# Kernel tuning notes

Measured on AMD Instinct MI355X. Metric: run time of the kernel, lower is better.

Reference implementation:

```python
import jax, jax.numpy as jnp
import numpy as np

B, N, H, OUT, L = 32, 4096, 256, 256, 4
EPS = 1e-5


def _build_edge_index(num_nodes):
    grid = int(np.sqrt(num_nodes)) + 1
    edges = []
    for i in range(num_nodes):
        col = i % grid
        if col < grid - 1 and i + 1 < num_nodes:
            edges.append([i, i + 1]); edges.append([i + 1, i])
        if i + grid < num_nodes:
            edges.append([i, i + grid]); edges.append([i + grid, i])
    return np.asarray(edges, dtype=np.int64).T  # [2, E]


def setup_inputs() -> dict:
    key = jax.random.key(0)
    ks = jax.random.split(key, 12)
    s = 0.02
    x = (jax.random.uniform(ks[0], (B, N)) < 0.1).astype(jnp.float32)  # syndrome bits
    edge_index = jnp.asarray(_build_edge_index(N))
    return {
        "x": x,
        "edge_index": edge_index,
        "proj_w": jax.random.normal(ks[1], (1, H)) * s,
        "proj_b": jnp.zeros((H,)),
        "conv_w": jax.random.normal(ks[2], (L, H, H)) * s,
        "conv_b": jnp.zeros((L, H)),
        "ln_g": jnp.ones((L, H)),
        "ln_b": jnp.zeros((L, H)),
        "h1_w": jax.random.normal(ks[3], (H, H)) * s,
        "h1_b": jnp.zeros((H,)),
        "h2_w": jax.random.normal(ks[4], (H, OUT)) * s,
        "h2_b": jnp.zeros((OUT,)),
    }


def reference(x, edge_index, proj_w, proj_b, conv_w, conv_b, ln_g, ln_b,
              h1_w, h1_b, h2_w, h2_b):
    batch, n = x.shape
    total = batch * n
    # batched edge index: replicate per sample with node offsets
    offsets = (jnp.arange(batch, dtype=edge_index.dtype) * n)
    ei = (edge_index[:, None, :] + offsets[None, :, None]).reshape(2, -1)
    src, dst = ei[0], ei[1]

    h = x.reshape(total, 1) @ proj_w + proj_b  # [total, H]

    # GCN symmetric norm with self-loops (degree = in-degree + 1)
    deg = jnp.zeros((total,), h.dtype).at[dst].add(1.0) + 1.0
    dinv_sqrt = jax.lax.rsqrt(deg)
    enorm = (dinv_sqrt[src] * dinv_sqrt[dst])[:, None]  # [E, 1]
    self_norm = (1.0 / deg)[:, None]                    # [total, 1]

    for l in range(L):
        t = h @ conv_w[l]                                   # transform
        agg = jnp.zeros_like(t).at[dst].add(enorm * t[src])  # scatter-add
        t = agg + self_norm * t + conv_b[l]
        mu = t.mean(-1, keepdims=True)
        var = ((t - mu) ** 2).mean(-1, keepdims=True)
        t = (t - mu) * jax.lax.rsqrt(var + EPS) * ln_g[l] + ln_b[l]
        h = jax.nn.relu(t)

    pooled = h.reshape(batch, n, -1).mean(axis=1)  # global_mean_pool (equal-size graphs)
    return jax.nn.relu(pooled @ h1_w + h1_b) @ h2_w + h2_b
```

## Files before the change

kernel.cpp:

```cpp
#include <hip/hip_runtime.h>
#include <cstdint>
#include <cstddef>

#define TOTAL (32*4096)
#define H 256
#define NLAYER 4

typedef __bf16 bf16x8 __attribute__((ext_vector_type(8)));
typedef float floatx4 __attribute__((ext_vector_type(4)));

__device__ __forceinline__ float u2f(unsigned int i) {
  union { unsigned int u; float f; } p; p.u = i; return p.f;
}
__device__ __forceinline__ float bf2f_lo(unsigned int u) { return u2f(u << 16); }
__device__ __forceinline__ float bf2f_hi(unsigned int u) { return u2f(u & 0xffff0000u); }
__device__ __forceinline__ unsigned int f2bf(float f) {
  union { float f; unsigned int i; } p; p.f = f;
  unsigned int r = p.i + 0x7fffu + ((p.i >> 16) & 1u);
  return r >> 16;
}

__device__ __forceinline__ float dinv_of(int n) {
  int col = n % 65;
  int deg = 1;
  deg += (n >= 1 && col != 0) ? 1 : 0;
  deg += (col != 64 && n <= 4094) ? 1 : 0;
  deg += (n >= 65) ? 1 : 0;
  deg += (n <= 4030) ? 1 : 0;
  return rsqrtf((float)deg);
}

__device__ __forceinline__ void load8(const unsigned short* p, float* v) {
  uint4 u = *reinterpret_cast<const uint4*>(p);
  v[0] = bf2f_lo(u.x); v[1] = bf2f_hi(u.x);
  v[2] = bf2f_lo(u.y); v[3] = bf2f_hi(u.y);
  v[4] = bf2f_lo(u.z); v[5] = bf2f_hi(u.z);
  v[6] = bf2f_lo(u.w); v[7] = bf2f_hi(u.w);
}
__device__ __forceinline__ uint4 pack8(const float* v) {
  uint4 u;
  u.x = f2bf(v[0]) | (f2bf(v[1]) << 16);
  u.y = f2bf(v[2]) | (f2bf(v[3]) << 16);
  u.z = f2bf(v[4]) | (f2bf(v[5]) << 16);
  u.w = f2bf(v[6]) | (f2bf(v[7]) << 16);
  return u;
}
__device__ __forceinline__ void loadf8(const float* p, float* v) {
  float4 a = *reinterpret_cast<const float4*>(p);
  float4 b = *reinterpret_cast<const float4*>(p + 4);
  v[0] = a.x; v[1] = a.y; v[2] = a.z; v[3] = a.w;
  v[4] = b.x; v[5] = b.y; v[6] = b.z; v[7] = b.w;
}

__global__ void k_transpose(const float* __restrict__ w,
                            unsigned short* __restrict__ wt,
                            float* __restrict__ pooled) {
  int idx = blockIdx.x * 256 + threadIdx.x;
  if (blockIdx.x < 32) pooled[idx] = 0.0f;
  int n = idx & 255;
  int k = (idx >> 8) & 255;
  int l = idx >> 16;
  int ngrp = n >> 4, ll = n & 15, c = k >> 5, lq = (k >> 3) & 3, j = k & 7;
  wt[(size_t)l * 65536 + (ngrp * 8 + c) * 512 + (lq * 16 + ll) * 8 + j] =
      (unsigned short)f2bf(w[idx]);
}

template <int AGG, int POOL, int GPROJ>
__global__ __launch_bounds__(256, 4)
void k_gemm_ln(const unsigned short* __restrict__ Hin,
               const float* __restrict__ x,
               const float* __restrict__ pw,
               const float* __restrict__ pb,
               const unsigned short* __restrict__ Bf,
               const float* __restrict__ cb,
               const float* __restrict__ lg,
               const float* __restrict__ lb,
               unsigned short* __restrict__ Hout,
               float* __restrict__ pooled) {
  __shared__ alignas(16) unsigned char smem_u[64 * 130 * 4];
  unsigned short* As = reinterpret_cast<unsigned short*>(smem_u);
  float*          p2 = reinterpret_cast<float*>(smem_u);
  __shared__ float red2[4][64][2];
  __shared__ float musr[64][2];
  const int t = threadIdx.x;
  const int w = t >> 6, lane = t & 63;
  const int lq = lane >> 4, ll = lane & 15;
  const int tile = (blockIdx.x & 7) * (gridDim.x >> 3) + (blockIdx.x >> 3);
  const int m0 = tile * 64;
  const int wc = w * 64;
  const int ar = t >> 2;
  const int ak = (t & 3) * 8;

  {
    const int gi = m0 + ar;
    const int nd = gi & 4095;
    const int col = nd % 65;
    const float di = dinv_of(nd);
    if (GPROJ) {
      const int base = gi - nd;
      float sx = di * x[gi];
      float sc = di;
      if (nd >= 1 && col != 0)     { float dj = dinv_of(nd - 1);  sx += dj * x[base + nd - 1];  sc += dj; }
      if (col != 64 && nd <= 4094) { float dj = dinv_of(nd + 1);  sx += dj * x[base + nd + 1];  sc += dj; }
      if (nd >= 65)                { float dj = dinv_of(nd - 65); sx += dj * x[base + nd - 65]; sc += dj; }
      if (nd <= 4030)              { float dj = dinv_of(nd + 65); sx += dj * x[base + nd + 65]; sc += dj; }
      sx *= di; sc *= di;
#pragma unroll
      for (int c = 0; c < 8; c++) {
        const int k0 = c * 32 + ak;
        float wv[8], bv[8], o[8];
        loadf8(pw + k0, wv);
        loadf8(pb + k0, bv);
#pragma unroll
        for (int q = 0; q < 8; q++) o[q] = sx * wv[q] + sc * bv[q];
        *reinterpret_cast<uint4*>(&As[c * 2048 + ar * 32 + ak]) = pack8(o);
      }
    } else if (AGG) {
      int j1 = gi, j2 = gi, j3 = gi, j4 = gi;
      float w1 = 0.f, w2 = 0.f, w3 = 0.f, w4 = 0.f;
      if (nd >= 1 && col != 0)     { j1 = gi - 1;  w1 = dinv_of(nd - 1); }
      if (col != 64 && nd <= 4094) { j2 = gi + 1;  w2 = dinv_of(nd + 1); }
      if (nd >= 65)                { j3 = gi - 65; w3 = dinv_of(nd - 65); }
      if (nd <= 4030)              { j4 = gi + 65; w4 = dinv_of(nd + 65); }
      const unsigned short* r0p = Hin + (size_t)gi * 256 + ak;
      const unsigned short* r1p = Hin + (size_t)j1 * 256 + ak;
      const unsigned short* r2p = Hin + (size_t)j2 * 256 + ak;
      const unsigned short* r3p = Hin + (size_t)j3 * 256 + ak;
      const unsigned short* r4p = Hin + (size_t)j4 * 256 + ak;
#pragma unroll
      for (int c = 0; c < 8; c++) {
        const int k0 = c * 32;
        float a0[8], a1[8], a2[8], a3[8], a4[8];
        load8(r0p + k0, a0);
        load8(r1p + k0, a1);
        load8(r2p + k0, a2);
        load8(r3p + k0, a3);
        load8(r4p + k0, a4);
        float o[8];
#pragma unroll
        for (int q = 0; q < 8; q++)
          o[q] = di * (di * a0[q] + w1 * a1[q] + w2 * a2[q] + w3 * a3[q] + w4 * a4[q]);
        *reinterpret_cast<uint4*>(&As[c * 2048 + ar * 32 + ak]) = pack8(o);
      }
    } else {
      const unsigned short* r0p = Hin + (size_t)gi * 256 + ak;
#pragma unroll
      for (int c = 0; c < 8; c++)
        *reinterpret_cast<uint4*>(&As[c * 2048 + ar * 32 + ak]) =
            *reinterpret_cast<const uint4*>(r0p + c * 32);
    }
  }
  __syncthreads();

  floatx4 acc[4][4] = {};
  const unsigned short* bbase = Bf + (size_t)(w * 4) * 8 * 512 + lane * 8;

#pragma unroll
  for (int c = 0; c < 8; c++) {
    bf16x8 bfr[4], af[4];
#pragma unroll
    for (int cc = 0; cc < 4; cc++)
      bfr[cc] = *reinterpret_cast<const bf16x8*>(bbase + (cc * 8 + c) * 512);
#pragma unroll
    for (int r = 0; r < 4; r++)
      af[r] = *reinterpret_cast<const bf16x8*>(&As[c * 2048 + (r * 16 + ll) * 32 + lq * 8]);
#pragma unroll
    for (int r = 0; r < 4; r++)
#pragma unroll
      for (int cc = 0; cc < 4; cc++)
        acc[r][cc] = __builtin_amdgcn_mfma_f32_16x16x32_bf16(af[r], bfr[cc], acc[r][cc], 0, 0, 0);
  }

  float cbv[4], gamv[4], betv[4];
#pragma unroll
  for (int c = 0; c < 4; c++) {
    int colc = wc + c * 16 + ll;
    cbv[c] = cb[colc]; gamv[c] = lg[colc]; betv[c] = lb[colc];
  }

  __syncthreads();
  {
    const int slice2 = (w * 16 + ll) * 2;
#pragma unroll
    for (int r = 0; r < 4; r++) {
#pragma unroll
      for (int reg = 0; reg < 4; reg++) {
        float sv = 0.f, sq = 0.f;
#pragma unroll
        for (int c = 0; c < 4; c++) {
          float v = acc[r][c][reg] + cbv[c];
          sv += v; sq += v * v;
        }
        const int row = r * 16 + lq * 4 + reg;
        *reinterpret_cast<float2*>(&p2[row * 130 + slice2]) = make_float2(sv, sq);
      }
    }
  }
  __syncthreads();
  {
    const int row = t & 63, qu = t >> 6;
    float s = 0.f, q = 0.f;
#pragma unroll
    for (int i = 0; i < 16; i++) {
      float2 pq = *reinterpret_cast<const float2*>(&p2[row * 130 + (qu * 16 + i) * 2]);
      s += pq.x; q += pq.y;
    }
    red2[qu][row][0] = s;
    red2[qu][row][1] = q;
  }
  __syncthreads();
  if (t < 64) {
    float s = red2[0][t][0] + red2[1][t][0] + red2[2][t][0] + red2[3][t][0];
    float q = red2[0][t][1] + red2[1][t][1] + red2[2][t][1] + red2[3][t][1];
    float mu = s * (1.0f / 256.0f);
    float var = fmaxf(q * (1.0f / 256.0f) - mu * mu, 0.0f);
    musr[t][0] = mu;
    musr[t][1] = rsqrtf(var + 1e-5f);
  }
  __syncthreads();

  if (POOL == 0) {
#pragma unroll
    for (int r = 0; r < 4; r++) {
#pragma unroll
      for (int reg = 0; reg < 4; reg++) {
        int row = r * 16 + lq * 4 + reg;
        float mu = musr[row][0], rs = musr[row][1];
#pragma unroll
        for (int c = 0; c < 4; c++) {
          float hv = (acc[r][c][reg] + cbv[c] - mu) * rs * gamv[c] + betv[c];
          hv = fmaxf(hv, 0.0f);
          Hout[(size_t)(m0 + row) * 256 + wc + c * 16 + ll] = (unsigned short)f2bf(hv);
        }
      }
    }
  } else {
    float csum[4] = {0.f, 0.f, 0.f, 0.f};
#pragma unroll
    for (int r = 0; r < 4; r++) {
#pragma unroll
      for (int reg = 0; reg < 4; reg++) {
        int row = r * 16 + lq * 4 + reg;
        float mu = musr[row][0], rs = musr[row][1];
#pragma unroll
        for (int c = 0; c < 4; c++) {
          float hv = (acc[r][c][reg] + cbv[c] - mu) * rs * gamv[c] + betv[c];
          csum[c] += fmaxf(hv, 0.0f);
        }
      }
    }
#pragma unroll
    for (int c = 0; c < 4; c++) {
      csum[c] += __shfl_xor(csum[c], 16, 64);
      csum[c] += __shfl_xor(csum[c], 32, 64);
    }
    if (lq == 0) {
      int b = m0 >> 12;
#pragma unroll
      for (int c = 0; c < 4; c++)
        atomicAdd(&pooled[b * 256 + wc + c * 16 + ll], csum[c] * (1.0f / 4096.0f));
    }
  }
}

__global__ void k_head(const float* __restrict__ pooled,
                       const float* __restrict__ w1,
                       const float* __restrict__ b1,
                       const float* __restrict__ w2,
                       const float* __restrict__ b2,
                       float* __restrict__ out) {
  const int b = blockIdx.x;
  const int t = threadIdx.x;
  __shared__ float row[256];
  __shared__ float y1[256];
  row[t] = pooled[b * 256 + t];
  __syncthreads();
  float s = b1[t];
#pragma unroll 8
  for (int k = 0; k < 256; k++) s += row[k] * w1[k * 256 + t];
  y1[t] = fmaxf(s, 0.0f);
  __syncthreads();
  float s2 = b2[t];
#pragma unroll 8
  for (int k = 0; k < 256; k++) s2 += y1[k] * w2[k * 256 + t];
  out[b * 256 + t] = s2;
}

extern "C" void kernel_launch(void* const* d_in, const int* in_sizes, int n_in,
                              void* d_out, int out_size, void* d_ws, size_t ws_size,
                              hipStream_t stream) {
  (void)in_sizes; (void)n_in; (void)out_size; (void)ws_size;
  const float* x      = (const float*)d_in[0];
  const float* proj_w = (const float*)d_in[2];
  const float* proj_b = (const float*)d_in[3];
  const float* conv_w = (const float*)d_in[4];
  const float* conv_b = (const float*)d_in[5];
  const float* ln_g   = (const float*)d_in[6];
  const float* ln_b   = (const float*)d_in[7];
  const float* h1_w   = (const float*)d_in[8];
  const float* h1_b   = (const float*)d_in[9];
  const float* h2_w   = (const float*)d_in[10];
  const float* h2_b   = (const float*)d_in[11];

  char* ws = (char*)d_ws;
  const size_t act_bytes = (size_t)TOTAL * H * 2;
  unsigned short* ha     = (unsigned short*)ws;
  unsigned short* hb     = (unsigned short*)(ws + act_bytes);
  unsigned short* wt     = (unsigned short*)(ws + 2 * act_bytes);
  float*          pooled = (float*)(ws + 2 * act_bytes + (size_t)NLAYER * H * H * 2);

  k_transpose<<<NLAYER * H * H / 256, 256, 0, stream>>>(conv_w, wt, pooled);

  const int GB = TOTAL / 64;
  k_gemm_ln<0, 0, 1><<<GB, 256, 0, stream>>>(nullptr, x, proj_w, proj_b,
      wt + 0 * (size_t)H * H, conv_b + 0 * H, ln_g + 0 * H, ln_b + 0 * H, hb, nullptr);
  k_gemm_ln<1, 0, 0><<<GB, 256, 0, stream>>>(hb, nullptr, nullptr, nullptr,
      wt + 1 * (size_t)H * H, conv_b + 1 * H, ln_g + 1 * H, ln_b + 1 * H, ha, nullptr);
  k_gemm_ln<1, 0, 0><<<GB, 256, 0, stream>>>(ha, nullptr, nullptr, nullptr,
      wt + 2 * (size_t)H * H, conv_b + 2 * H, ln_g + 2 * H, ln_b + 2 * H, hb, nullptr);
  k_gemm_ln<1, 1, 0><<<GB, 256, 0, stream>>>(hb, nullptr, nullptr, nullptr,
      wt + 3 * (size_t)H * H, conv_b + 3 * H, ln_g + 3 * H, ln_b + 3 * H, nullptr, pooled);

  k_head<<<32, 256, 0, stream>>>(pooled, h1_w, h1_b, h2_w, h2_b, (float*)d_out);
}
```

Before: 259.9 us.

## Permute weight columns so each lane owns four contiguous outputs and stores packed bf16

Changes the pre-transposed weight layout so each MFMA lane's four column tiles map to four adjacent output columns. The epilogue can then load bias and LayerNorm parameters as float4 and write each row's four outputs as one 8-byte store instead of four scattered 2-byte stores. It also switches bf16 packing to the hardware v_cvt_pk_bf16_f32 instruction. The layout permutation must stay consistent with every consumer of the weights and of the output column indices, including the pooling atomics.

```diff
diff --git a/kernel.cpp b/kernel.cpp
--- a/kernel.cpp
+++ b/kernel.cpp
@@ -18,6 +18,11 @@
   union { float f; unsigned int i; } p; p.f = f;
   unsigned int r = p.i + 0x7fffu + ((p.i >> 16) & 1u);
   return r >> 16;
+}
+__device__ __forceinline__ unsigned int cvt_pk_bf16(float lo, float hi) {
+  unsigned int r;
+  asm("v_cvt_pk_bf16_f32 %0, %1, %2" : "=v"(r) : "v"(lo), "v"(hi));
+  return r;
 }
 
 __device__ __forceinline__ float dinv_of(int n) {
@@ -39,10 +44,10 @@
 }
 __device__ __forceinline__ uint4 pack8(const float* v) {
   uint4 u;
-  u.x = f2bf(v[0]) | (f2bf(v[1]) << 16);
-  u.y = f2bf(v[2]) | (f2bf(v[3]) << 16);
-  u.z = f2bf(v[4]) | (f2bf(v[5]) << 16);
-  u.w = f2bf(v[6]) | (f2bf(v[7]) << 16);
+  u.x = cvt_pk_bf16(v[0], v[1]);
+  u.y = cvt_pk_bf16(v[2], v[3]);
+  u.z = cvt_pk_bf16(v[4], v[5]);
+  u.w = cvt_pk_bf16(v[6], v[7]);
   return u;
 }
 __device__ __forceinline__ void loadf8(const float* p, float* v) {
@@ -52,7 +57,7 @@
   v[4] = b.x; v[5] = b.y; v[6] = b.z; v[7] = b.w;
 }
 
-__global__ void k_transpose(const float* __restrict__ w,
+__global__ void k_transpose(const float* __restrict__ src,
                             unsigned short* __restrict__ wt,
                             float* __restrict__ pooled) {
   int idx = blockIdx.x * 256 + threadIdx.x;
@@ -60,9 +65,11 @@
   int n = idx & 255;
   int k = (idx >> 8) & 255;
   int l = idx >> 16;
-  int ngrp = n >> 4, ll = n & 15, c = k >> 5, lq = (k >> 3) & 3, j = k & 7;
+  int wgrp = n >> 6, cc = n & 3, ll = (n >> 2) & 15;
+  int ngrp = wgrp * 4 + cc;
+  int c = k >> 5, lq = (k >> 3) & 3, j = k & 7;
   wt[(size_t)l * 65536 + (ngrp * 8 + c) * 512 + (lq * 16 + ll) * 8 + j] =
-      (unsigned short)f2bf(w[idx]);
+      (unsigned short)f2bf(src[idx]);
 }
 
 template <int AGG, int POOL, int GPROJ>
@@ -171,12 +178,13 @@
         acc[r][cc] = __builtin_amdgcn_mfma_f32_16x16x32_bf16(af[r], bfr[cc], acc[r][cc], 0, 0, 0);
   }
 
-  float cbv[4], gamv[4], betv[4];
-#pragma unroll
-  for (int c = 0; c < 4; c++) {
-    int colc = wc + c * 16 + ll;
-    cbv[c] = cb[colc]; gamv[c] = lg[colc]; betv[c] = lb[colc];
-  }
+  const int colbase = wc + (ll << 2);
+  const float4 cb4 = *reinterpret_cast<const float4*>(cb + colbase);
+  const float4 lg4 = *reinterpret_cast<const float4*>(lg + colbase);
+  const float4 lb4 = *reinterpret_cast<const float4*>(lb + colbase);
+  const float cbv[4]  = {cb4.x, cb4.y, cb4.z, cb4.w};
+  const float gamv[4] = {lg4.x, lg4.y, lg4.z, lg4.w};
+  const float betv[4] = {lb4.x, lb4.y, lb4.z, lb4.w};
 
   __syncthreads();
   {
@@ -226,12 +234,16 @@
       for (int reg = 0; reg < 4; reg++) {
         int row = r * 16 + lq * 4 + reg;
         float mu = musr[row][0], rs = musr[row][1];
+        float hv[4];
 #pragma unroll
         for (int c = 0; c < 4; c++) {
-          float hv = (acc[r][c][reg] + cbv[c] - mu) * rs * gamv[c] + betv[c];
-          hv = fmaxf(hv, 0.0f);
-          Hout[(size_t)(m0 + row) * 256 + wc + c * 16 + ll] = (unsigned short)f2bf(hv);
+          float v = (acc[r][c][reg] + cbv[c] - mu) * rs * gamv[c] + betv[c];
+          hv[c] = fmaxf(v, 0.0f);
         }
+        uint2 st;
+        st.x = cvt_pk_bf16(hv[0], hv[1]);
+        st.y = cvt_pk_bf16(hv[2], hv[3]);
+        *reinterpret_cast<uint2*>(&Hout[(size_t)(m0 + row) * 256 + colbase]) = st;
       }
     }
   } else {
@@ -258,7 +270,7 @@
       int b = m0 >> 12;
 #pragma unroll
       for (int c = 0; c < 4; c++)
-        atomicAdd(&pooled[b * 256 + wc + c * 16 + ll], csum[c] * (1.0f / 4096.0f));
+        atomicAdd(&pooled[b * 256 + colbase + c], csum[c] * (1.0f / 4096.0f));
     }
   }
 }
```

Result: slower. 273.8 us (+5.3%).
